# Performance work log

Measured on AMD Instinct MI355X. Metric: run time of the kernel, lower is better.

Reference implementation:

```python
import jax, jax.numpy as jnp
import numpy as np

N = 50000          # total residues (nodes)
E = 800000         # contact edges, avg degree 16
F_IN = 1280        # ESM embedding dim
H = 256            # hidden
L = 4              # num_layers
B = 100            # proteins in batch
MAX_NODES = 500    # residues per protein (uniform -> static to_dense_batch shape)


def setup_inputs() -> dict:
    key = jax.random.key(0)
    ks = jax.random.split(key, 16)
    s = 0.02
    inp = {
        "seq": jax.random.randint(ks[0], (N,), 0, 26),
        "edge_index": jax.random.randint(ks[1], (2, E), 0, N),
        "esm_token": jax.random.normal(ks[2], (N, F_IN), jnp.float32),
        "batch": jnp.arange(N) // MAX_NODES,
        # lin0
        "lin0_W": jax.random.normal(ks[3], (F_IN, H), jnp.float32) * s,
        "lin0_b": jnp.zeros((H,), jnp.float32),
        # WeightConv1 per layer: lin1 (root), lin2 (neighbor), lin3 (mask head)
        "wc_W1": jax.random.normal(ks[4], (L, H, H), jnp.float32) * s,
        "wc_b1": jnp.zeros((L, H), jnp.float32),
        "wc_W2": jax.random.normal(ks[5], (L, H, H), jnp.float32) * s,
        "wc_b2": jnp.zeros((L, H), jnp.float32),
        "wc_W3": jax.random.normal(ks[6], (L, H, H), jnp.float32) * s,
        "wc_b3": jnp.zeros((L, H), jnp.float32),
        # SparseConv per layer: neighbor weight + bias, root weight
        "sc_Wn": jax.random.normal(ks[7], (L, H, H), jnp.float32) * s,
        "sc_bn": jnp.zeros((L, H), jnp.float32),
        "sc_Wr": jax.random.normal(ks[8], (L, H, H), jnp.float32) * s,
    }
    return inp


def reference(seq, edge_index, esm_token, batch,
              lin0_W, lin0_b,
              wc_W1, wc_b1, wc_W2, wc_b2, wc_W3, wc_b3,
              sc_Wn, sc_bn, sc_Wr):
    src, dst = edge_index[0], edge_index[1]
    x = esm_token @ lin0_W + lin0_b              # [N, H]
    mask_val = None
    xs = []
    for i in range(L):
        # ---- WeightConv1: learned edge-conditioned node mask ----
        xm = x if mask_val is None else x * mask_val
        h_nb = xm @ wc_W2[i] + wc_b2[i]          # neighbor transform [N, H]
        agg = jax.ops.segment_sum(h_nb[src], dst, num_segments=N)
        h = jax.nn.relu(agg + xm @ wc_W1[i] + wc_b1[i])
        mask_val = jax.nn.sigmoid(h @ wc_W3[i] + wc_b3[i])   # [N, H]
        # ---- SparseConv: mask-gated sparse aggregation ----
        xg = x * mask_val
        agg2 = jax.ops.segment_sum(xg[src], dst, num_segments=N)
        x = jax.nn.relu(agg2 @ sc_Wn[i] + sc_bn[i] + x @ sc_Wr[i])
        xs.append(x)
    feat = jnp.concatenate(xs, axis=-1)          # jumping-knowledge cat [N, L*H]
    # ---- to_dense_batch ----
    counts = jax.ops.segment_sum(jnp.ones((N,), jnp.int32), batch, num_segments=B)
    starts = jnp.cumsum(counts) - counts
    pos = jnp.arange(N) - starts[batch]
    dense = jnp.zeros((B, MAX_NODES, L * H), feat.dtype).at[batch, pos].set(feat)
    node_mask = jnp.zeros((B, MAX_NODES), bool).at[batch, pos].set(True)
    return dense, node_mask
```

## Files before the change

### kernel.cpp

```cpp
#include <hip/hip_runtime.h>

#define NNODES 50000
#define HDIM 256
#define NLAYERS 4
#define NEDGES 800000
#define FIN 1280
#define LDOUT 1024

typedef _Float16 f16;
typedef __attribute__((ext_vector_type(8))) _Float16 f16x8;
typedef __attribute__((ext_vector_type(4))) _Float16 f16x4;
typedef __attribute__((ext_vector_type(4))) float f32x4;


__global__ __launch_bounds__(256) void hm_k(
    const f16*  __restrict__ aggx,
    const f16*  __restrict__ xm,
    const f16*  __restrict__ xh,
    const int*  __restrict__ deg,
    const f16*  __restrict__ WH,
    const f16*  __restrict__ W3t,
    const float* __restrict__ b2,
    const float* __restrict__ b1,
    const float* __restrict__ b3,
    f16* __restrict__ maskh,
    f16* __restrict__ xg)
{
    __shared__ f16 lds[16384];

    const int row0 = blockIdx.x * 64;
    const int tid = threadIdx.x;
    const int wv = tid >> 6;
    const int l = tid & 63;

    f32x4 acc[4][4] = {};

    const int sr = tid >> 2;
    const int sc0 = (tid & 3) * 16;
    const int grow = row0 + sr;
    const bool rok = grow < NNODES;
    const int lane_base0 =
        (((sc0 >> 5) * 4 + (sr >> 4)) * 64 + (sr & 15) + (((sc0 & 31) >> 3) * 16)) * 8;
    const int lane_base1 = lane_base0 + 128;

    const f16* bp[4];
    #pragma unroll
    for (int cf = 0; cf < 4; ++cf)
        bp[cf] = WH + (size_t)(wv * 64 + cf * 16 + (l & 15)) * 512 + ((l >> 4) * 8);

    struct SReg { f16x8 h0, h1; };
    SReg RA, RB;

    auto LOAD = [&](SReg& r, int kt) {
        if (!rok) return;
        const int k0 = kt * 64 + sc0;
        const f16* p = (k0 < HDIM) ? (aggx + (size_t)grow * HDIM + k0)
                                   : (xm + (size_t)grow * HDIM + (k0 - HDIM));
        r.h0 = *(const f16x8*)p;  r.h1 = *(const f16x8*)(p + 8);
    };

    auto COMMIT = [&](const SReg& r, int b) {
        f16x8 av0, av1;
        #pragma unroll
        for (int i = 0; i < 8; ++i) { av0[i] = (f16)0.f; av1[i] = (f16)0.f; }
        if (rok) { av0 = r.h0; av1 = r.h1; }
        *(f16x8*)(&lds[b * 4096 + lane_base0]) = av0;
        *(f16x8*)(&lds[b * 4096 + lane_base1]) = av1;
    };

    auto TILE = [&](int b, int kt) {
        f16x8 af[4][2];
        #pragma unroll
        for (int rf = 0; rf < 4; ++rf)
            #pragma unroll
            for (int kb = 0; kb < 2; ++kb)
                af[rf][kb] = *(const f16x8*)(&lds[b * 4096 + ((kb * 4 + rf) * 64 + l) * 8]);
        f16x8 bfr[4][2];
        #pragma unroll
        for (int cf = 0; cf < 4; ++cf) {
            bfr[cf][0] = *(const f16x8*)(bp[cf] + kt * 64);
            bfr[cf][1] = *(const f16x8*)(bp[cf] + kt * 64 + 32);
        }
        #pragma unroll
        for (int cf = 0; cf < 4; ++cf)
            #pragma unroll
            for (int rf = 0; rf < 4; ++rf)
                #pragma unroll
                for (int kb = 0; kb < 2; ++kb)
                    acc[rf][cf] = __builtin_amdgcn_mfma_f32_16x16x32_f16(
                        af[rf][kb], bfr[cf][kb], acc[rf][cf], 0, 0, 0);
    };

    LOAD(RA, 0);
    COMMIT(RA, 0);
    LOAD(RB, 1);
    #pragma unroll
    for (int kt2 = 0; kt2 < 8; kt2 += 2) {
        __syncthreads();
        TILE(0, kt2);
        COMMIT(RB, 1);
        if (kt2 + 2 < 8) LOAD(RA, kt2 + 2);
        __syncthreads();
        TILE(1, kt2 + 1);
        if (kt2 + 2 < 8) COMMIT(RA, 0);
        if (kt2 + 3 < 8) LOAD(RB, kt2 + 3);
    }
    __syncthreads();

    #pragma unroll
    for (int rf = 0; rf < 4; ++rf) {
        #pragma unroll
        for (int j = 0; j < 4; ++j) {
            const int rowl = rf * 16 + ((l >> 4) * 4) + j;
            const int row = row0 + rowl;
            const float dv = (row < NNODES) ? (float)deg[row] : 0.f;
            #pragma unroll
            for (int cf = 0; cf < 4; ++cf) {
                const int col = wv * 64 + cf * 16 + (l & 15);
                const float h = fmaxf(acc[rf][cf][j] + dv * b2[col] + b1[col], 0.f);
                const int idx =
                    (((col >> 6) * 8 + ((col >> 5) & 1) * 4 + (rowl >> 4)) * 64
                     + ((col >> 3) & 3) * 16 + (rowl & 15)) * 8 + (col & 7);
                lds[idx] = (f16)h;
            }
        }
    }
    __syncthreads();

    const f16* bp3[4];
    #pragma unroll
    for (int cf = 0; cf < 4; ++cf)
        bp3[cf] = W3t + (size_t)(wv * 64 + cf * 16 + (l & 15)) * 256 + ((l >> 4) * 8);

    f32x4 acc2[4][4] = {};
    f16x8 bC[4][2], bN[4][2];
    #pragma unroll
    for (int cf = 0; cf < 4; ++cf) {
        bC[cf][0] = *(const f16x8*)(bp3[cf]);
        bC[cf][1] = *(const f16x8*)(bp3[cf] + 32);
    }
    #pragma unroll
    for (int kt = 0; kt < 4; ++kt) {
        if (kt < 3) {
            #pragma unroll
            for (int cf = 0; cf < 4; ++cf) {
                bN[cf][0] = *(const f16x8*)(bp3[cf] + (kt + 1) * 64);
                bN[cf][1] = *(const f16x8*)(bp3[cf] + (kt + 1) * 64 + 32);
            }
        }
        f16x8 af[4][2];
        #pragma unroll
        for (int rf = 0; rf < 4; ++rf)
            #pragma unroll
            for (int kb = 0; kb < 2; ++kb)
                af[rf][kb] = *(const f16x8*)(&lds[((kt * 8 + kb * 4 + rf) * 64 + l) * 8]);
        #pragma unroll
        for (int cf = 0; cf < 4; ++cf)
            #pragma unroll
            for (int rf = 0; rf < 4; ++rf)
                #pragma unroll
                for (int kb = 0; kb < 2; ++kb)
                    acc2[rf][cf] = __builtin_amdgcn_mfma_f32_16x16x32_f16(
                        af[rf][kb], bC[cf][kb], acc2[rf][cf], 0, 0, 0);
        if (kt < 3) {
            #pragma unroll
            for (int cf = 0; cf < 4; ++cf) {
                bC[cf][0] = bN[cf][0];  bC[cf][1] = bN[cf][1];
            }
        }
    }

    #pragma unroll
    for (int rf = 0; rf < 4; ++rf) {
        #pragma unroll
        for (int j = 0; j < 4; ++j) {
            const int row = row0 + rf * 16 + ((l >> 4) * 4) + j;
            if (row >= NNODES) continue;
            #pragma unroll
            for (int cf = 0; cf < 4; ++cf) {
                const int col = wv * 64 + cf * 16 + (l & 15);
                const float m = 1.f / (1.f + expf(-(acc2[rf][cf][j] + b3[col])));
                maskh[(size_t)row * HDIM + col] = (f16)m;
                xg[(size_t)row * HDIM + col] =
                    (f16)((float)xh[(size_t)row * HDIM + col] * m);
            }
        }
    }
}

__global__ __launch_bounds__(256) void cath2_k(
    const f16*  __restrict__ A3,
    const f16*  __restrict__ A4,
    const f16*  __restrict__ Mh,
    const f16*  __restrict__ Wt,
    const float* __restrict__ bias,
    float* __restrict__ Cf, int ldc,
    f16*  __restrict__ Ch,
    f16*  __restrict__ Ch3)
{
    constexpr int KTILES = 8;
    constexpr int K = 512;
    __shared__ f16 Asm[2][4096];

    const int row0 = blockIdx.x * 64;
    const int tid = threadIdx.x;
    const int wv = tid >> 6;
    const int l = tid & 63;

    f32x4 acc[4][4] = {};

    const int sr = tid >> 2;
    const int sc0 = (tid & 3) * 16;
    const int grow = row0 + sr;
    const bool rok = grow < NNODES;
    const int lane_base0 =
        (((sc0 >> 5) * 4 + (sr >> 4)) * 64 + (sr & 15) + (((sc0 & 31) >> 3) * 16)) * 8;
    const int lane_base1 = lane_base0 + 128;

    const f16* bp[4];
    #pragma unroll
    for (int cf = 0; cf < 4; ++cf)
        bp[cf] = Wt + (size_t)(wv * 64 + cf * 16 + (l & 15)) * K + ((l >> 4) * 8);

    struct SReg { f16x8 h0, h1; };
    SReg RA, RB;

    auto LOAD = [&](SReg& r, int kt) {
        if (!rok) return;
        const int k0 = kt * 64 + sc0;
        const f16* p = (k0 < HDIM) ? (A3 + (size_t)grow * HDIM + k0)
                                   : (A4 + (size_t)grow * HDIM + (k0 - HDIM));
        r.h0 = *(const f16x8*)p;  r.h1 = *(const f16x8*)(p + 8);
    };

    auto COMMIT = [&](const SReg& r, int b) {
        f16x8 av0, av1;
        #pragma unroll
        for (int i = 0; i < 8; ++i) { av0[i] = (f16)0.f; av1[i] = (f16)0.f; }
        if (rok) { av0 = r.h0; av1 = r.h1; }
        *(f16x8*)(&Asm[b][lane_base0]) = av0;
        *(f16x8*)(&Asm[b][lane_base1]) = av1;
    };

    auto TILE = [&](int b, int kt) {
        f16x8 af[4][2];
        #pragma unroll
        for (int rf = 0; rf < 4; ++rf)
            #pragma unroll
            for (int kb = 0; kb < 2; ++kb)
                af[rf][kb] = *(const f16x8*)(&Asm[b][((kb * 4 + rf) * 64 + l) * 8]);
        f16x8 bfr[4][2];
        #pragma unroll
        for (int cf = 0; cf < 4; ++cf) {
            bfr[cf][0] = *(const f16x8*)(bp[cf] + kt * 64);
            bfr[cf][1] = *(const f16x8*)(bp[cf] + kt * 64 + 32);
        }
        #pragma unroll
        for (int cf = 0; cf < 4; ++cf)
            #pragma unroll
            for (int rf = 0; rf < 4; ++rf)
                #pragma unroll
                for (int kb = 0; kb < 2; ++kb)
                    acc[rf][cf] = __builtin_amdgcn_mfma_f32_16x16x32_f16(
                        af[rf][kb], bfr[cf][kb], acc[rf][cf], 0, 0, 0);
    };

    LOAD(RA, 0);
    COMMIT(RA, 0);
    LOAD(RB, 1);
    #pragma unroll
    for (int kt2 = 0; kt2 < KTILES; kt2 += 2) {
        __syncthreads();
        TILE(0, kt2);
        COMMIT(RB, 1);
        if (kt2 + 2 < KTILES) LOAD(RA, kt2 + 2);
        __syncthreads();
        TILE(1, kt2 + 1);
        if (kt2 + 2 < KTILES) COMMIT(RA, 0);
        if (kt2 + 3 < KTILES) LOAD(RB, kt2 + 3);
    }

    #pragma unroll
    for (int rf = 0; rf < 4; ++rf) {
        #pragma unroll
        for (int j = 0; j < 4; ++j) {
            const int row = row0 + rf * 16 + ((l >> 4) * 4) + j;
            if (row >= NNODES) continue;
            #pragma unroll
            for (int cf = 0; cf < 4; ++cf) {
                const int col = wv * 64 + cf * 16 + (l & 15);
                const float r = fmaxf(acc[rf][cf][j] + bias[col], 0.f);
                Cf[(size_t)row * ldc + col] = r;
                Ch[(size_t)row * HDIM + col] = (f16)r;
                Ch3[(size_t)row * HDIM + col] =
                    (f16)(r * (float)Mh[(size_t)row * HDIM + col]);
            }
        }
    }
}

template<int KTILES>
__global__ __launch_bounds__(256) void lin0_k(
    const float* __restrict__ A1, int lda1,
    const f16*  __restrict__ WtBase,
    f16* __restrict__ parts)
{
    constexpr int K = KTILES * 64;
    __shared__ f16 Asm[2][4096];

    const int row0 = blockIdx.x * 64;
    const int by = blockIdx.y;
    const int tid = threadIdx.x;
    const int wv = tid >> 6;
    const int l = tid & 63;

    f32x4 acc[4][4] = {};

    const int sr = tid >> 2;
    const int sc0 = (tid & 3) * 16;
    const int grow = row0 + sr;
    const bool rok = grow < NNODES;
    const int kg = by * K;
    const int lane_base0 =
        (((sc0 >> 5) * 4 + (sr >> 4)) * 64 + (sr & 15) + (((sc0 & 31) >> 3) * 16)) * 8;
    const int lane_base1 = lane_base0 + 128;

    const f16* Wsel = WtBase + (size_t)by * 256 * K;
    const f16* bp[4];
    #pragma unroll
    for (int cf = 0; cf < 4; ++cf)
        bp[cf] = Wsel + (size_t)(wv * 64 + cf * 16 + (l & 15)) * K + ((l >> 4) * 8);

    struct SReg { float4 f0, f1, f2, f3; };
    SReg RA, RB;

    auto LOAD = [&](SReg& r, int kt) {
        if (!rok) return;
        const float* p = A1 + (size_t)grow * lda1 + kg + kt * 64 + sc0;
        r.f0 = *(const float4*)(p + 0);  r.f1 = *(const float4*)(p + 4);
        r.f2 = *(const float4*)(p + 8);  r.f3 = *(const float4*)(p + 12);
    };

    auto COMMIT = [&](const SReg& r, int b) {
        f16x8 av0, av1;
        #pragma unroll
        for (int i = 0; i < 8; ++i) { av0[i] = (f16)0.f; av1[i] = (f16)0.f; }
        if (rok) {
            av0[0]=(f16)r.f0.x; av0[1]=(f16)r.f0.y; av0[2]=(f16)r.f0.z; av0[3]=(f16)r.f0.w;
            av0[4]=(f16)r.f1.x; av0[5]=(f16)r.f1.y; av0[6]=(f16)r.f1.z; av0[7]=(f16)r.f1.w;
            av1[0]=(f16)r.f2.x; av1[1]=(f16)r.f2.y; av1[2]=(f16)r.f2.z; av1[3]=(f16)r.f2.w;
            av1[4]=(f16)r.f3.x; av1[5]=(f16)r.f3.y; av1[6]=(f16)r.f3.z; av1[7]=(f16)r.f3.w;
        }
        *(f16x8*)(&Asm[b][lane_base0]) = av0;
        *(f16x8*)(&Asm[b][lane_base1]) = av1;
    };

    auto TILE = [&](int b, int kt) {
        f16x8 af[4][2];
        #pragma unroll
        for (int rf = 0; rf < 4; ++rf)
            #pragma unroll
            for (int kb = 0; kb < 2; ++kb)
                af[rf][kb] = *(const f16x8*)(&Asm[b][((kb * 4 + rf) * 64 + l) * 8]);
        f16x8 bfr[4][2];
        #pragma unroll
        for (int cf = 0; cf < 4; ++cf) {
            bfr[cf][0] = *(const f16x8*)(bp[cf] + kt * 64);
            bfr[cf][1] = *(const f16x8*)(bp[cf] + kt * 64 + 32);
        }
        #pragma unroll
        for (int cf = 0; cf < 4; ++cf)
            #pragma unroll
            for (int rf = 0; rf < 4; ++rf)
                #pragma unroll
                for (int kb = 0; kb < 2; ++kb)
                    acc[rf][cf] = __builtin_amdgcn_mfma_f32_16x16x32_f16(
                        af[rf][kb], bfr[cf][kb], acc[rf][cf], 0, 0, 0);
    };

    LOAD(RA, 0);
    COMMIT(RA, 0);
    if (KTILES > 1) LOAD(RB, 1);
    #pragma unroll
    for (int kt2 = 0; kt2 < KTILES; kt2 += 2) {
        __syncthreads();
        TILE(0, kt2);
        if (kt2 + 1 < KTILES) COMMIT(RB, 1);
        if (kt2 + 2 < KTILES) LOAD(RA, kt2 + 2);
        if (kt2 + 1 < KTILES) {
            __syncthreads();
            TILE(1, kt2 + 1);
            if (kt2 + 2 < KTILES) COMMIT(RA, 0);
            if (kt2 + 3 < KTILES) LOAD(RB, kt2 + 3);
        }
    }

    f16* Ph = parts + (size_t)by * NNODES * HDIM;
    #pragma unroll
    for (int rf = 0; rf < 4; ++rf) {
        #pragma unroll
        for (int j = 0; j < 4; ++j) {
            const int row = row0 + rf * 16 + ((l >> 4) * 4) + j;
            if (row >= NNODES) continue;
            #pragma unroll
            for (int cf = 0; cf < 4; ++cf) {
                const int col = wv * 64 + cf * 16 + (l & 15);
                Ph[(size_t)row * HDIM + col] = (f16)acc[rf][cf][j];
            }
        }
    }
}

__global__ __launch_bounds__(256) void combine4_k(
    const f16* __restrict__ parts, const float* __restrict__ b,
    f16* __restrict__ xh)
{
    const int t = blockIdx.x * 256 + threadIdx.x;
    const int row = t >> 6;
    const int c = (t & 63) * 4;
    if (row >= NNODES) return;
    const size_t NH = (size_t)NNODES * HDIM;
    const size_t off = (size_t)row * HDIM + c;
    f16x4 p0 = *(const f16x4*)(parts + off);
    f16x4 p1 = *(const f16x4*)(parts + NH + off);
    f16x4 p2 = *(const f16x4*)(parts + 2 * NH + off);
    f16x4 p3 = *(const f16x4*)(parts + 3 * NH + off);
    const float4 bb = *(const float4*)(b + c);
    f16x4 r;
    r[0] = (f16)((float)p0[0] + (float)p1[0] + (float)p2[0] + (float)p3[0] + bb.x);
    r[1] = (f16)((float)p0[1] + (float)p1[1] + (float)p2[1] + (float)p3[1] + bb.y);
    r[2] = (f16)((float)p0[2] + (float)p1[2] + (float)p2[2] + (float)p3[2] + bb.z);
    r[3] = (f16)((float)p0[3] + (float)p1[3] + (float)p2[3] + (float)p3[3] + bb.w);
    *(f16x4*)(xh + off) = r;
}

__global__ __launch_bounds__(256) void pack_all_k(
    const float* __restrict__ lin0_W,
    const float* __restrict__ W2, const float* __restrict__ W1,
    const float* __restrict__ W3,
    const float* __restrict__ Wn, const float* __restrict__ Wr,
    f16* __restrict__ dst)
{
    int idx = blockIdx.x * 256 + threadIdx.x;
    const int total = 327680 + 524288 + 262144 + 524288;
    if (idx >= total) return;
    f16* d = dst + idx;
    if (idx < 327680) {
        const int q = idx / 81920;
        int r = idx % 81920;
        const int col = r / 320, k = r % 320;
        *d = (f16)lin0_W[(size_t)(k + q * 320) * 256 + col];
        return;
    }
    idx -= 327680;
    if (idx < 524288) {
        const int i = idx / 131072;
        int r = idx % 131072;
        const int col = r / 512, k = r % 512;
        *d = (f16)(k < 256 ? W2[(size_t)i * 65536 + k * 256 + col]
                           : W1[(size_t)i * 65536 + (k - 256) * 256 + col]);
        return;
    }
    idx -= 524288;
    if (idx < 262144) {
        const int i = idx / 65536;
        int r = idx % 65536;
        const int col = r / 256, k = r % 256;
        *d = (f16)W3[(size_t)i * 65536 + k * 256 + col];
        return;
    }
    idx -= 262144;
    const int i = idx / 131072; int r = idx % 131072;
    const int col = r / 512, k = r % 512;
    *d = (f16)(k < 256 ? Wn[(size_t)i * 65536 + k * 256 + col]
                       : Wr[(size_t)i * 65536 + (k - 256) * 256 + col]);
}

__global__ __launch_bounds__(256) void count_k(
    const int* __restrict__ dstIdx, int* __restrict__ counts)
{
    const int e = blockIdx.x * 256 + threadIdx.x;
    if (e < NEDGES) atomicAdd(&counts[dstIdx[e]], 1);
}

__global__ __launch_bounds__(1024) void scan_k(
    const int* __restrict__ counts, int* __restrict__ starts)
{
    __shared__ int sm[1024];
    __shared__ int s_off;
    if (threadIdx.x == 0) s_off = 0;
    __syncthreads();
    for (int base = 0; base < NNODES; base += 1024) {
        const int i = base + threadIdx.x;
        const int v = (i < NNODES) ? counts[i] : 0;
        sm[threadIdx.x] = v;
        __syncthreads();
        for (int ofs = 1; ofs < 1024; ofs <<= 1) {
            const int t = (threadIdx.x >= ofs) ? sm[threadIdx.x - ofs] : 0;
            __syncthreads();
            sm[threadIdx.x] += t;
            __syncthreads();
        }
        const int incl = sm[threadIdx.x];
        const int off = s_off;
        if (i < NNODES) starts[i] = off + incl - v;
        __syncthreads();
        if (threadIdx.x == 1023) s_off = off + incl;
        __syncthreads();
    }
    if (threadIdx.x == 0) starts[NNODES] = s_off;
}

__global__ __launch_bounds__(256) void fillcsr_k(
    const int* __restrict__ srcIdx, const int* __restrict__ dstIdx,
    int* __restrict__ cursor, int* __restrict__ csr)
{
    const int e = blockIdx.x * 256 + threadIdx.x;
    if (e >= NEDGES) return;
    const int d = dstIdx[e];
    const int p = atomicAdd(&cursor[d], 1);
    csr[p] = srcIdx[e];
}

__global__ __launch_bounds__(256) void gather_g_k(
    const f16* __restrict__ rows, const int* __restrict__ csr,
    const int* __restrict__ starts, f16* __restrict__ outp)
{
    const int node = (blockIdx.x * 256 + threadIdx.x) >> 6;
    const int lane = threadIdx.x & 63;
    if (node >= NNODES) return;
    const int e0 = starts[node], e1 = starts[node + 1];
    float a0=0,a1=0,a2=0,a3=0, b0=0,b1=0,b2=0,b3=0;
    int e = e0;
    for (; e + 3 < e1; e += 4) {
        const int s0=csr[e], s1=csr[e+1], s2=csr[e+2], s3=csr[e+3];
        f16x4 v0 = *(const f16x4*)(rows + (size_t)s0 * HDIM + lane * 4);
        f16x4 v1 = *(const f16x4*)(rows + (size_t)s1 * HDIM + lane * 4);
        f16x4 v2 = *(const f16x4*)(rows + (size_t)s2 * HDIM + lane * 4);
        f16x4 v3 = *(const f16x4*)(rows + (size_t)s3 * HDIM + lane * 4);
        a0 += (float)v0[0] + (float)v2[0]; a1 += (float)v0[1] + (float)v2[1];
        a2 += (float)v0[2] + (float)v2[2]; a3 += (float)v0[3] + (float)v2[3];
        b0 += (float)v1[0] + (float)v3[0]; b1 += (float)v1[1] + (float)v3[1];
        b2 += (float)v1[2] + (float)v3[2]; b3 += (float)v1[3] + (float)v3[3];
    }
    for (; e < e1; ++e) {
        const int s0 = csr[e];
        f16x4 v0 = *(const f16x4*)(rows + (size_t)s0 * HDIM + lane * 4);
        a0 += (float)v0[0]; a1 += (float)v0[1]; a2 += (float)v0[2]; a3 += (float)v0[3];
    }
    f16x4 r;
    r[0] = (f16)(a0 + b0); r[1] = (f16)(a1 + b1);
    r[2] = (f16)(a2 + b2); r[3] = (f16)(a3 + b3);
    *(f16x4*)(outp + (size_t)node * HDIM + lane * 4) = r;
}

__global__ __launch_bounds__(256) void fill1_k(float* __restrict__ p, int n)
{
    const int t = blockIdx.x * 256 + threadIdx.x;
    if (t < n) p[t] = 1.0f;
}

extern "C" void kernel_launch(void* const* d_in, const int* in_sizes, int n_in,
                              void* d_out, int out_size, void* d_ws, size_t ws_size,
                              hipStream_t stream)
{
    const int*   edge   = (const int*)d_in[1];
    const int*   src    = edge;
    const int*   dst    = edge + NEDGES;
    const float* esm    = (const float*)d_in[2];
    const float* lin0_W = (const float*)d_in[4];
    const float* lin0_b = (const float*)d_in[5];
    const float* wc_W1  = (const float*)d_in[6];
    const float* wc_b1  = (const float*)d_in[7];
    const float* wc_W2  = (const float*)d_in[8];
    const float* wc_b2  = (const float*)d_in[9];
    const float* wc_W3  = (const float*)d_in[10];
    const float* wc_b3  = (const float*)d_in[11];
    const float* sc_Wn  = (const float*)d_in[12];
    const float* sc_bn  = (const float*)d_in[13];
    const float* sc_Wr  = (const float*)d_in[14];
    float* out = (float*)d_out;

    const size_t NH = (size_t)NNODES * HDIM;
    f16* parts = (f16*)d_ws;
    f16* aggx  = parts;
    f16* xg    = parts + NH;
    f16* agg2  = parts + 2 * NH;
    f16* xh    = parts + 4 * NH;
    f16* xm    = xh + NH;
    f16* maskh = xm + NH;
    f16* wpack = maskh + NH;
    f16* lin0t = wpack;
    f16* WH    = lin0t + 327680;
    f16* W3t   = WH + 524288;
    f16* WtC   = W3t + 262144;
    int* iws    = (int*)(WtC + 524288);
    int* counts = iws;
    int* starts = iws + NNODES;
    int* cursor = iws + 2 * NNODES + 1;
    int* csr    = iws + 3 * NNODES + 2;

    const dim3 blk(256);
    const int gemmGrid = (NNODES + 63) / 64;
    const int edgeGrid = (NEDGES + 255) / 256;
    const int waveGrid = (NNODES * 64) / 256;

    hipMemsetAsync(counts, 0, NNODES * sizeof(int), stream);
    count_k<<<edgeGrid, blk, 0, stream>>>(dst, counts);
    scan_k<<<1, 1024, 0, stream>>>(counts, starts);
    hipMemcpyAsync(cursor, starts, NNODES * sizeof(int),
                   hipMemcpyDeviceToDevice, stream);
    fillcsr_k<<<edgeGrid, blk, 0, stream>>>(src, dst, cursor, csr);

    pack_all_k<<<(1638400 + 255) / 256, blk, 0, stream>>>(
        lin0_W, wc_W2, wc_W1, wc_W3, sc_Wn, sc_Wr, wpack);

    lin0_k<5><<<dim3(gemmGrid, 4), blk, 0, stream>>>(esm, FIN, lin0t, parts);
    combine4_k<<<waveGrid, blk, 0, stream>>>(parts, lin0_b, xh);

    for (int i = 0; i < NLAYERS; ++i) {
        const size_t bo = (size_t)i * HDIM;
        const f16* wh = WH + (size_t)i * 131072;
        const f16* w3 = W3t + (size_t)i * 65536;
        const f16* wc = WtC + (size_t)i * 131072;
        const f16* xmtab = (i == 0) ? xh : xm;

        gather_g_k<<<waveGrid, blk, 0, stream>>>(xmtab, csr, starts, aggx);
        hm_k<<<gemmGrid, blk, 0, stream>>>(
            aggx, xmtab, xh, counts, wh, w3,
            wc_b2 + bo, wc_b1 + bo, wc_b3 + bo, maskh, xg);
        gather_g_k<<<waveGrid, blk, 0, stream>>>(xg, csr, starts, agg2);
        cath2_k<<<gemmGrid, blk, 0, stream>>>(
            agg2, xh, maskh, wc, sc_bn + bo,
            out + (size_t)i * HDIM, LDOUT, xh, xm);
    }

    const size_t maskOff = (size_t)NNODES * LDOUT;
    fill1_k<<<(NNODES + 255) / 256, blk, 0, stream>>>(out + maskOff, NNODES);
}
```

Baseline: 1.312 ms.

## Load GEMM A fragments directly from global memory instead of staging through LDS

In both the fused mask-head kernel and the SparseConv GEMM kernel, the A-operand tiles are no longer double-buffered through shared memory with barriers. Each wave now loads its MFMA A fragments straight from global memory in the fragment layout. The W3 prefetch double-buffer in the second GEMM is also dropped. This removes LDS traffic and per-tile __syncthreads, but all four waves now read the same A rows redundantly from global memory or L2, and software prefetch of the next tile is lost.

```diff
diff --git a/kernel.cpp b/kernel.cpp
--- a/kernel.cpp
+++ b/kernel.cpp
@@ -26,60 +26,49 @@
     f16* __restrict__ maskh,
     f16* __restrict__ xg)
 {
-    __shared__ f16 lds[16384];
+    __shared__ f16 Hfr[16384];
 
     const int row0 = blockIdx.x * 64;
     const int tid = threadIdx.x;
     const int wv = tid >> 6;
     const int l = tid & 63;
+    const int ak = (l >> 4) * 8;
+
+    int arow[4]; bool av[4];
+    #pragma unroll
+    for (int rf = 0; rf < 4; ++rf) {
+        arow[rf] = row0 + rf * 16 + (l & 15);
+        av[rf] = arow[rf] < NNODES;
+    }
+
+    const f16* bp[4];
+    #pragma unroll
+    for (int cf = 0; cf < 4; ++cf)
+        bp[cf] = WH + (size_t)(wv * 64 + cf * 16 + (l & 15)) * 512 + ak;
 
     f32x4 acc[4][4] = {};
 
-    const int sr = tid >> 2;
-    const int sc0 = (tid & 3) * 16;
-    const int grow = row0 + sr;
-    const bool rok = grow < NNODES;
-    const int lane_base0 =
-        (((sc0 >> 5) * 4 + (sr >> 4)) * 64 + (sr & 15) + (((sc0 & 31) >> 3) * 16)) * 8;
-    const int lane_base1 = lane_base0 + 128;
-
-    const f16* bp[4];
-    #pragma unroll
-    for (int cf = 0; cf < 4; ++cf)
-        bp[cf] = WH + (size_t)(wv * 64 + cf * 16 + (l & 15)) * 512 + ((l >> 4) * 8);
-
-    struct SReg { f16x8 h0, h1; };
-    SReg RA, RB;
-
-    auto LOAD = [&](SReg& r, int kt) {
-        if (!rok) return;
-        const int k0 = kt * 64 + sc0;
-        const f16* p = (k0 < HDIM) ? (aggx + (size_t)grow * HDIM + k0)
-                                   : (xm + (size_t)grow * HDIM + (k0 - HDIM));
-        r.h0 = *(const f16x8*)p;  r.h1 = *(const f16x8*)(p + 8);
-    };
-
-    auto COMMIT = [&](const SReg& r, int b) {
-        f16x8 av0, av1;
-        #pragma unroll
-        for (int i = 0; i < 8; ++i) { av0[i] = (f16)0.f; av1[i] = (f16)0.f; }
-        if (rok) { av0 = r.h0; av1 = r.h1; }
-        *(f16x8*)(&lds[b * 4096 + lane_base0]) = av0;
-        *(f16x8*)(&lds[b * 4096 + lane_base1]) = av1;
-    };
-
-    auto TILE = [&](int b, int kt) {
+    #pragma unroll
+    for (int kt = 0; kt < 8; ++kt) {
+        const f16* base = (kt < 4) ? aggx : xm;
+        const int koff = (kt & 3) * 64 + ak;
         f16x8 af[4][2];
         #pragma unroll
         for (int rf = 0; rf < 4; ++rf)
             #pragma unroll
-            for (int kb = 0; kb < 2; ++kb)
-                af[rf][kb] = *(const f16x8*)(&lds[b * 4096 + ((kb * 4 + rf) * 64 + l) * 8]);
-        f16x8 bfr[4][2];
+            for (int kb = 0; kb < 2; ++kb) {
+                f16x8 v;
+                #pragma unroll
+                for (int i = 0; i < 8; ++i) v[i] = (f16)0.f;
+                if (av[rf])
+                    v = *(const f16x8*)(base + (size_t)arow[rf] * HDIM + koff + kb * 32);
+                af[rf][kb] = v;
+            }
+        f16x8 bf[4][2];
         #pragma unroll
         for (int cf = 0; cf < 4; ++cf) {
-            bfr[cf][0] = *(const f16x8*)(bp[cf] + kt * 64);
-            bfr[cf][1] = *(const f16x8*)(bp[cf] + kt * 64 + 32);
+            bf[cf][0] = *(const f16x8*)(bp[cf] + kt * 64);
+            bf[cf][1] = *(const f16x8*)(bp[cf] + kt * 64 + 32);
         }
         #pragma unroll
         for (int cf = 0; cf < 4; ++cf)
@@ -88,24 +77,8 @@
                 #pragma unroll
                 for (int kb = 0; kb < 2; ++kb)
                     acc[rf][cf] = __builtin_amdgcn_mfma_f32_16x16x32_f16(
-                        af[rf][kb], bfr[cf][kb], acc[rf][cf], 0, 0, 0);
-    };
-
-    LOAD(RA, 0);
-    COMMIT(RA, 0);
-    LOAD(RB, 1);
-    #pragma unroll
-    for (int kt2 = 0; kt2 < 8; kt2 += 2) {
-        __syncthreads();
-        TILE(0, kt2);
-        COMMIT(RB, 1);
-        if (kt2 + 2 < 8) LOAD(RA, kt2 + 2);
-        __syncthreads();
-        TILE(1, kt2 + 1);
-        if (kt2 + 2 < 8) COMMIT(RA, 0);
-        if (kt2 + 3 < 8) LOAD(RB, kt2 + 3);
-    }
-    __syncthreads();
+                        af[rf][kb], bf[cf][kb], acc[rf][cf], 0, 0, 0);
+    }
 
     #pragma unroll
     for (int rf = 0; rf < 4; ++rf) {
@@ -121,7 +94,7 @@
                 const int idx =
                     (((col >> 6) * 8 + ((col >> 5) & 1) * 4 + (rowl >> 4)) * 64
                      + ((col >> 3) & 3) * 16 + (rowl & 15)) * 8 + (col & 7);
-                lds[idx] = (f16)h;
+                Hfr[idx] = (f16)h;
             }
         }
     }
@@ -130,30 +103,23 @@
     const f16* bp3[4];
     #pragma unroll
     for (int cf = 0; cf < 4; ++cf)
-        bp3[cf] = W3t + (size_t)(wv * 64 + cf * 16 + (l & 15)) * 256 + ((l >> 4) * 8);
+        bp3[cf] = W3t + (size_t)(wv * 64 + cf * 16 + (l & 15)) * 256 + ak;
 
     f32x4 acc2[4][4] = {};
-    f16x8 bC[4][2], bN[4][2];
-    #pragma unroll
-    for (int cf = 0; cf < 4; ++cf) {
-        bC[cf][0] = *(const f16x8*)(bp3[cf]);
-        bC[cf][1] = *(const f16x8*)(bp3[cf] + 32);
-    }
     #pragma unroll
     for (int kt = 0; kt < 4; ++kt) {
-        if (kt < 3) {
-            #pragma unroll
-            for (int cf = 0; cf < 4; ++cf) {
-                bN[cf][0] = *(const f16x8*)(bp3[cf] + (kt + 1) * 64);
-                bN[cf][1] = *(const f16x8*)(bp3[cf] + (kt + 1) * 64 + 32);
-            }
-        }
         f16x8 af[4][2];
         #pragma unroll
         for (int rf = 0; rf < 4; ++rf)
             #pragma unroll
             for (int kb = 0; kb < 2; ++kb)
-                af[rf][kb] = *(const f16x8*)(&lds[((kt * 8 + kb * 4 + rf) * 64 + l) * 8]);
+                af[rf][kb] = *(const f16x8*)(&Hfr[((kt * 8 + kb * 4 + rf) * 64 + l) * 8]);
+        f16x8 bf[4][2];
+        #pragma unroll
+        for (int cf = 0; cf < 4; ++cf) {
+            bf[cf][0] = *(const f16x8*)(bp3[cf] + kt * 64);
+            bf[cf][1] = *(const f16x8*)(bp3[cf] + kt * 64 + 32);
+        }
         #pragma unroll
         for (int cf = 0; cf < 4; ++cf)
             #pragma unroll
@@ -161,13 +127,7 @@
                 #pragma unroll
                 for (int kb = 0; kb < 2; ++kb)
                     acc2[rf][cf] = __builtin_amdgcn_mfma_f32_16x16x32_f16(
-                        af[rf][kb], bC[cf][kb], acc2[rf][cf], 0, 0, 0);
-        if (kt < 3) {
-            #pragma unroll
-            for (int cf = 0; cf < 4; ++cf) {
-                bC[cf][0] = bN[cf][0];  bC[cf][1] = bN[cf][1];
-            }
-        }
+                        af[rf][kb], bf[cf][kb], acc2[rf][cf], 0, 0, 0);
     }
 
     #pragma unroll
@@ -189,8 +149,8 @@
 }
 
 __global__ __launch_bounds__(256) void cath2_k(
-    const f16*  __restrict__ A3,
-    const f16*  __restrict__ A4,
+    const f16*  __restrict__ agg2,
+    const f16*  __restrict__ xh,
     const f16*  __restrict__ Mh,
     const f16*  __restrict__ Wt,
     const float* __restrict__ bias,
@@ -198,62 +158,47 @@
     f16*  __restrict__ Ch,
     f16*  __restrict__ Ch3)
 {
-    constexpr int KTILES = 8;
-    constexpr int K = 512;
-    __shared__ f16 Asm[2][4096];
-
     const int row0 = blockIdx.x * 64;
     const int tid = threadIdx.x;
     const int wv = tid >> 6;
     const int l = tid & 63;
+    const int ak = (l >> 4) * 8;
+
+    int arow[4]; bool av[4];
+    #pragma unroll
+    for (int rf = 0; rf < 4; ++rf) {
+        arow[rf] = row0 + rf * 16 + (l & 15);
+        av[rf] = arow[rf] < NNODES;
+    }
+
+    const f16* bp[4];
+    #pragma unroll
+    for (int cf = 0; cf < 4; ++cf)
+        bp[cf] = Wt + (size_t)(wv * 64 + cf * 16 + (l & 15)) * 512 + ak;
 
     f32x4 acc[4][4] = {};
 
-    const int sr = tid >> 2;
-    const int sc0 = (tid & 3) * 16;
-    const int grow = row0 + sr;
-    const bool rok = grow < NNODES;
-    const int lane_base0 =
-        (((sc0 >> 5) * 4 + (sr >> 4)) * 64 + (sr & 15) + (((sc0 & 31) >> 3) * 16)) * 8;
-    const int lane_base1 = lane_base0 + 128;
-
-    const f16* bp[4];
-    #pragma unroll
-    for (int cf = 0; cf < 4; ++cf)
-        bp[cf] = Wt + (size_t)(wv * 64 + cf * 16 + (l & 15)) * K + ((l >> 4) * 8);
-
-    struct SReg { f16x8 h0, h1; };
-    SReg RA, RB;
-
-    auto LOAD = [&](SReg& r, int kt) {
-        if (!rok) return;
-        const int k0 = kt * 64 + sc0;
-        const f16* p = (k0 < HDIM) ? (A3 + (size_t)grow * HDIM + k0)
-                                   : (A4 + (size_t)grow * HDIM + (k0 - HDIM));
-        r.h0 = *(const f16x8*)p;  r.h1 = *(const f16x8*)(p + 8);
-    };
-
-    auto COMMIT = [&](const SReg& r, int b) {
-        f16x8 av0, av1;
-        #pragma unroll
-        for (int i = 0; i < 8; ++i) { av0[i] = (f16)0.f; av1[i] = (f16)0.f; }
-        if (rok) { av0 = r.h0; av1 = r.h1; }
-        *(f16x8*)(&Asm[b][lane_base0]) = av0;
-        *(f16x8*)(&Asm[b][lane_base1]) = av1;
-    };
-
-    auto TILE = [&](int b, int kt) {
+    #pragma unroll
+    for (int kt = 0; kt < 8; ++kt) {
+        const f16* base = (kt < 4) ? agg2 : xh;
+        const int koff = (kt & 3) * 64 + ak;
         f16x8 af[4][2];
         #pragma unroll
         for (int rf = 0; rf < 4; ++rf)
             #pragma unroll
-            for (int kb = 0; kb < 2; ++kb)
-                af[rf][kb] = *(const f16x8*)(&Asm[b][((kb * 4 + rf) * 64 + l) * 8]);
-        f16x8 bfr[4][2];
+            for (int kb = 0; kb < 2; ++kb) {
+                f16x8 v;
+                #pragma unroll
+                for (int i = 0; i < 8; ++i) v[i] = (f16)0.f;
+                if (av[rf])
+                    v = *(const f16x8*)(base + (size_t)arow[rf] * HDIM + koff + kb * 32);
+                af[rf][kb] = v;
+            }
+        f16x8 bf[4][2];
         #pragma unroll
         for (int cf = 0; cf < 4; ++cf) {
-            bfr[cf][0] = *(const f16x8*)(bp[cf] + kt * 64);
-            bfr[cf][1] = *(const f16x8*)(bp[cf] + kt * 64 + 32);
+            bf[cf][0] = *(const f16x8*)(bp[cf] + kt * 64);
+            bf[cf][1] = *(const f16x8*)(bp[cf] + kt * 64 + 32);
         }
         #pragma unroll
         for (int cf = 0; cf < 4; ++cf)
@@ -262,23 +207,10 @@
                 #pragma unroll
                 for (int kb = 0; kb < 2; ++kb)
                     acc[rf][cf] = __builtin_amdgcn_mfma_f32_16x16x32_f16(
-                        af[rf][kb], bfr[cf][kb], acc[rf][cf], 0, 0, 0);
-    };
-
-    LOAD(RA, 0);
-    COMMIT(RA, 0);
-    LOAD(RB, 1);
-    #pragma unroll
-    for (int kt2 = 0; kt2 < KTILES; kt2 += 2) {
-        __syncthreads();
-        TILE(0, kt2);
-        COMMIT(RB, 1);
-        if (kt2 + 2 < KTILES) LOAD(RA, kt2 + 2);
-        __syncthreads();
-        TILE(1, kt2 + 1);
-        if (kt2 + 2 < KTILES) COMMIT(RA, 0);
-        if (kt2 + 3 < KTILES) LOAD(RB, kt2 + 3);
-    }
+                        af[rf][kb], bf[cf][kb], acc[rf][cf], 0, 0, 0);
+    }
+
+    __syncthreads();
 
     #pragma unroll
     for (int rf = 0; rf < 4; ++rf) {
```

New measurement: 1.493 ms. +13.7%, slower.
